# Kernel tuning notes

Hardware: AMD Instinct MI355X
Metric: run time of the kernel (lower is better)

## Reference

```python
import jax, jax.numpy as jnp
import numpy as np
import math

B, T, C = 4, 2048, 1024
H = 16
DH = C // H
SCALE = 1.0 / math.sqrt(DH)


def setup_inputs() -> dict:
    key = jax.random.key(0)
    k1, k2, k3 = jax.random.split(key, 3)
    x = jax.random.normal(k1, (B, T, C), dtype=jnp.float32)
    # init_unit_norm: randn / sqrt(d_in)
    W_qkv = jax.random.normal(k2, (3 * C, C), dtype=jnp.float32) / math.sqrt(C)
    W_out = jax.random.normal(k3, (C, C), dtype=jnp.float32) / math.sqrt(C)
    return {"x": x, "W_qkv": W_qkv, "W_out": W_out}


def reference(x, W_qkv, W_out):
    b, t, c = x.shape
    qkv = x @ W_qkv.T                      # [B,T,3C]
    q, k, v = jnp.split(qkv, 3, axis=-1)
    # [B,T,C] -> [B,H,T,Dh]
    q = q.reshape(b, t, H, DH).transpose(0, 2, 1, 3)
    k = k.reshape(b, t, H, DH).transpose(0, 2, 1, 3)
    v = v.reshape(b, t, H, DH).transpose(0, 2, 1, 3)
    scores = jnp.einsum('bhtd,bhsd->bhts', q, k) * SCALE  # [B,H,T,T]
    mask = jnp.tril(jnp.ones((t, t), dtype=bool))
    scores = jnp.where(mask, scores, 0.0)  # no softmax
    attn = jnp.einsum('bhts,bhsd->bhtd', scores, v)       # [B,H,T,Dh]
    attn = attn.transpose(0, 2, 1, 3).reshape(b, t, c)
    return attn @ W_out.T
```

## Files before the change

### kernel.cpp

```cpp
#include <hip/hip_runtime.h>

#define TT 2048
#define CC 1024

typedef __attribute__((ext_vector_type(8))) __bf16 bf16x8;
typedef __attribute__((ext_vector_type(4))) float f32x4;
typedef unsigned int u32;

__device__ __forceinline__ short f2bf(float f) {
  u32 u = __float_as_uint(f);
  u += 0x7fffu + ((u >> 16) & 1u);
  return (short)(u >> 16);
}

#if __has_builtin(__builtin_amdgcn_cvt_pk_bf16_f32)
__device__ __forceinline__ u32 pack2(float a, float b) {
  auto v = __builtin_amdgcn_cvt_pk_bf16_f32(a, b);
  return __builtin_bit_cast(u32, v);
}
#else
__device__ __forceinline__ u32 pack2(float a, float b) {
  u32 ua = __float_as_uint(a), ub = __float_as_uint(b);
  ua += 0x7fffu + ((ua >> 16) & 1u);
  ub += 0x7fffu + ((ub >> 16) & 1u);
  return (ua >> 16) | (ub & 0xffff0000u);
}
#endif

__global__ __launch_bounds__(256) void cvt_all(const float* __restrict__ x,
                                               const float* __restrict__ wqkv,
                                               const float* __restrict__ wout,
                                               short* __restrict__ dst) {
  int i = blockIdx.x * blockDim.x + threadIdx.x;
  const float* src;
  float sc = 1.0f;
  if (i < 2097152) {
    src = x + (size_t)i * 4;
  } else if (i < 2883584) {
    int j = i - 2097152;
    src = wqkv + (size_t)j * 4;
    if (j < 262144) sc = 0.125f;
  } else {
    src = wout + (size_t)(i - 2883584) * 4;
  }
  float4 f = *reinterpret_cast<const float4*>(src);
  short4 s;
  s.x = f2bf(f.x * sc); s.y = f2bf(f.y * sc); s.z = f2bf(f.z * sc); s.w = f2bf(f.w * sc);
  reinterpret_cast<short4*>(dst)[i] = s;
}

__device__ __forceinline__ void storev(float* p, float v) { *p = v; }
__device__ __forceinline__ void storev(short* p, float v) { *p = f2bf(v); }

#if __has_builtin(__builtin_amdgcn_global_load_lds)
#define HAVE_GLD_LDS 1
__device__ __forceinline__ void gld_lds16(const short* g, short* l) {
  __builtin_amdgcn_global_load_lds((const __attribute__((address_space(1))) u32*)g,
                                   (__attribute__((address_space(3))) u32*)l, 16, 0, 0);
}
#endif

__device__ __forceinline__ f32x4 mfma16(bf16x8 a, bf16x8 b, f32x4 c) {
  return __builtin_amdgcn_mfma_f32_16x16x32_bf16(a, b, c, 0, 0, 0);
}

template <int NN>
__device__ __forceinline__ void waitvm() {
  if constexpr (NN == 0) asm volatile("s_waitcnt vmcnt(0)" ::: "memory");
  else if constexpr (NN == 4) asm volatile("s_waitcnt vmcnt(4)" ::: "memory");
  else if constexpr (NN == 6) asm volatile("s_waitcnt vmcnt(6)" ::: "memory");
  else if constexpr (NN == 8) asm volatile("s_waitcnt vmcnt(8)" ::: "memory");
}

template <int MH, int NFR>
__device__ __forceinline__ void mmaN(f32x4 (&acc)[8][NFR], const bf16x8 (&af)[4],
                                     const bf16x8 (&bfr)[NFR]) {
#pragma unroll
  for (int mf = 0; mf < 4; ++mf)
#pragma unroll
    for (int nf = 0; nf < NFR; ++nf)
      acc[MH * 4 + mf][nf] = mfma16(af[mf], bfr[nf], acc[MH * 4 + mf][nf]);
}

#define GPHASE(DB, KS, MH, LOADB, STG, SYNC)               \
  {                                                        \
    ldA(af, DB, KS, MH);                                   \
    if (LOADB) ldB(bfr, DB, KS);                           \
    STG;                                                   \
    __builtin_amdgcn_s_setprio(1);                         \
    mmaN<MH>(acc, af, bfr);                                \
    __builtin_amdgcn_s_setprio(0);                         \
    asm volatile("s_waitcnt lgkmcnt(0)" ::: "memory");     \
    SYNC;                                                  \
    __builtin_amdgcn_s_barrier();                          \
  }
#define GNOOP ((void)0)

template <typename OutT, int N, int K, int BN, int RN>
__global__ __launch_bounds__(512, 2) void gemm8p(const short* __restrict__ A,
                                                 const short* __restrict__ B,
                                                 OutT* __restrict__ Cm) {
  constexpr int BGLD = BN / 128;
  constexpr int NFR = BN / 64;
  constexpr int SYNCN = 2 + 2 * BGLD;
  constexpr int NT = K / 64, NITER = NT / 2;
  constexpr int BHALF = BN * 32;
  constexpr int DBS = 16384 + BN * 64;
  extern __shared__ short lds[];
  const int tid = threadIdx.x;
  const int wave = tid >> 6, lane = tid & 63;
  const int quad = lane >> 4, nl = lane & 15;
  const int wm = wave >> 2, wn = wave & 3;

  const int id = blockIdx.x;
  const int xcd = id & 7, slot = id >> 3;
  const int mt = (xcd & 3) * 8 + (slot & 7);
  const int nt = (xcd >> 2) * RN + (slot >> 3);
  const int m0 = mt * 256, n0 = nt * BN;

  const int srow = lane >> 2;
  const int sperm = ((lane & 3) ^ ((lane >> 3) & 3)) * 8;
  const short* pA = A + (size_t)(m0 + wave * 32 + srow) * K + sperm;
  const short* pB = B + (size_t)(n0 + wave * (BN / 8) + srow) * K + sperm;

  const int perm = (quad ^ ((nl >> 1) & 3)) * 8;
  const int aoff = (wm * 128 + nl) * 32 + perm;
  const int boff = (wn * (BN / 4) + nl) * 32 + perm;

  f32x4 acc[8][NFR] = {};

  auto stageA = [&](int db, int ks, int t) {
    const short* s = pA + (size_t)t * 64 + ks * 32;
    short* d = lds + db * DBS + ks * 8192 + wave * 1024;
#if HAVE_GLD_LDS
    gld_lds16(s, d);
    gld_lds16(s + (size_t)16 * K, d + 512);
#else
    *reinterpret_cast<uint4*>(d + lane * 8) = *reinterpret_cast<const uint4*>(s);
    *reinterpret_cast<uint4*>(d + 512 + lane * 8) =
        *reinterpret_cast<const uint4*>(s + (size_t)16 * K);
#endif
  };
  auto stageB = [&](int db, int ks, int t) {
    const short* s = pB + (size_t)t * 64 + ks * 32;
    short* d = lds + db * DBS + 16384 + ks * BHALF + wave * (BN * 4);
#if HAVE_GLD_LDS
    gld_lds16(s, d);
    if constexpr (BGLD == 2) gld_lds16(s + (size_t)16 * K, d + 512);
#else
    *reinterpret_cast<uint4*>(d + lane * 8) = *reinterpret_cast<const uint4*>(s);
    if constexpr (BGLD == 2)
      *reinterpret_cast<uint4*>(d + 512 + lane * 8) =
          *reinterpret_cast<const uint4*>(s + (size_t)16 * K);
#endif
  };
  auto ldA = [&](bf16x8 (&af)[4], int db, int ks, int mh) {
#pragma unroll
    for (int mf = 0; mf < 4; ++mf)
      af[mf] = *reinterpret_cast<const bf16x8*>(
          &lds[db * DBS + ks * 8192 + aoff + (mh * 4 + mf) * 512]);
  };
  auto ldB = [&](bf16x8 (&bfr)[NFR], int db, int ks) {
#pragma unroll
    for (int nf = 0; nf < NFR; ++nf)
      bfr[nf] = *reinterpret_cast<const bf16x8*>(
          &lds[db * DBS + 16384 + ks * BHALF + boff + nf * 512]);
  };

  stageA(0, 0, 0); stageA(0, 1, 0); stageB(0, 0, 0); stageB(0, 1, 0);
  stageB(1, 0, 1); stageA(1, 0, 1); stageB(1, 1, 1);
  waitvm<SYNCN>();
  __builtin_amdgcn_s_barrier();

  for (int i = 0; i < NITER - 1; ++i) {
    const int to1 = 2 * i + 1, te2 = 2 * i + 2, to3 = 2 * i + 3;
    bf16x8 af[4], bfr[NFR];
    GPHASE(0, 0, 0, 1, stageA(1, 1, to1), GNOOP)
    GPHASE(0, 0, 1, 0, stageB(0, 0, te2), GNOOP)
    GPHASE(0, 1, 0, 1, stageA(0, 0, te2), GNOOP)
    GPHASE(0, 1, 1, 0, stageB(0, 1, te2), waitvm<SYNCN>())
    GPHASE(1, 0, 0, 1, stageA(0, 1, te2), GNOOP)
    GPHASE(1, 0, 1, 0, stageB(1, 0, to3), GNOOP)
    GPHASE(1, 1, 0, 1, stageA(1, 0, to3), GNOOP)
    GPHASE(1, 1, 1, 0, stageB(1, 1, to3), waitvm<SYNCN>())
  }
  {
    bf16x8 af[4], bfr[NFR];
    GPHASE(0, 0, 0, 1, stageA(1, 1, NT - 1), GNOOP)
    GPHASE(0, 0, 1, 0, GNOOP, GNOOP)
    GPHASE(0, 1, 0, 1, GNOOP, GNOOP)
    GPHASE(0, 1, 1, 0, GNOOP, waitvm<0>())
    GPHASE(1, 0, 0, 1, GNOOP, GNOOP)
    GPHASE(1, 0, 1, 0, GNOOP, GNOOP)
    GPHASE(1, 1, 0, 1, GNOOP, GNOOP)
    GPHASE(1, 1, 1, 0, GNOOP, GNOOP)
  }

#pragma unroll
  for (int mf = 0; mf < 8; ++mf) {
    const int row = m0 + wm * 128 + mf * 16 + quad * 4;
#pragma unroll
    for (int nf = 0; nf < NFR; ++nf) {
      const int col = n0 + wn * (BN / 4) + nf * 16 + nl;
#pragma unroll
      for (int r = 0; r < 4; ++r)
        storev(&Cm[(size_t)(row + r) * N + col], acc[mf][nf][r]);
    }
  }
}

__global__ __launch_bounds__(256) void transpose_v(const short* __restrict__ qkv,
                                                   short* __restrict__ vt) {
  __shared__ short Ls[64 * 68];
  const int bh = blockIdx.y, tb = blockIdx.x;
  const int b = bh >> 4, h = bh & 15;
  const int tid = threadIdx.x;
  const short* src = qkv + (size_t)(b * TT + tb * 64) * (3 * CC) + 2 * CC + h * 64;
#pragma unroll
  for (int i = 0; i < 2; ++i) {
    int idx = tid + i * 256;
    int tl = idx >> 3, dc = idx & 7;
    uint4 d4 = *reinterpret_cast<const uint4*>(&src[(size_t)tl * (3 * CC) + dc * 8]);
    *reinterpret_cast<uint2*>(&Ls[tl * 68 + dc * 8]) = make_uint2(d4.x, d4.y);
    *reinterpret_cast<uint2*>(&Ls[tl * 68 + dc * 8 + 4]) = make_uint2(d4.z, d4.w);
  }
  __syncthreads();
  short* dst = vt + (size_t)(bh * 64) * TT + tb * 64;
#pragma unroll
  for (int i = 0; i < 2; ++i) {
    int idx = tid + i * 256;
    int dl = idx >> 3, tc = idx & 7;
    short tmp[8];
#pragma unroll
    for (int j = 0; j < 8; ++j) tmp[j] = Ls[(tc * 8 + j) * 68 + dl];
    *reinterpret_cast<uint4*>(&dst[(size_t)dl * TT + tc * 8]) = *reinterpret_cast<uint4*>(tmp);
  }
}

template <bool DIAG>
__device__ __forceinline__ void attn_compute(const short* kf, const short* vf, u32* ssw,
                                             const bf16x8 (&qf)[2][2], f32x4 (&o)[2][4],
                                             int lane, int quad, int nl) {
  bf16x8 k00 = *reinterpret_cast<const bf16x8*>(&kf[0 * 512 + lane * 8]);
  bf16x8 k01 = *reinterpret_cast<const bf16x8*>(&kf[1 * 512 + lane * 8]);
  bf16x8 k10 = *reinterpret_cast<const bf16x8*>(&kf[2 * 512 + lane * 8]);
  bf16x8 k11 = *reinterpret_cast<const bf16x8*>(&kf[3 * 512 + lane * 8]);
  bf16x8 vB[4];
#pragma unroll
  for (int nb = 0; nb < 4; ++nb)
    vB[nb] = *reinterpret_cast<const bf16x8*>(&vf[nb * 512 + lane * 8]);
  {
    u32* srow = &ssw[0 * 320 + nl * 20];
    f32x4 s0 = {};
    s0 = mfma16(k00, qf[0][0], s0);
    s0 = mfma16(k01, qf[0][1], s0);
    if (DIAG) {
#pragma unroll
      for (int r = 0; r < 4; ++r) s0[r] = (quad * 4 + r <= nl) ? s0[r] : 0.0f;
    }
#pragma unroll
    for (int p = 0; p < 2; ++p) srow[quad * 2 + p] = pack2(s0[2 * p], s0[2 * p + 1]);
    if (DIAG) {
#pragma unroll
      for (int p = 0; p < 2; ++p) srow[8 + quad * 2 + p] = 0;
    } else {
      f32x4 s1 = {};
      s1 = mfma16(k10, qf[0][0], s1);
      s1 = mfma16(k11, qf[0][1], s1);
#pragma unroll
      for (int p = 0; p < 2; ++p) srow[8 + quad * 2 + p] = pack2(s1[2 * p], s1[2 * p + 1]);
    }
  }
  {
    u32* srow = &ssw[1 * 320 + nl * 20];
    f32x4 s0 = {}, s1 = {};
    s0 = mfma16(k00, qf[1][0], s0);
    s0 = mfma16(k01, qf[1][1], s0);
    s1 = mfma16(k10, qf[1][0], s1);
    s1 = mfma16(k11, qf[1][1], s1);
    if (DIAG) {
#pragma unroll
      for (int r = 0; r < 4; ++r) s1[r] = (quad * 4 + r <= nl) ? s1[r] : 0.0f;
    }
#pragma unroll
    for (int p = 0; p < 2; ++p) {
      srow[quad * 2 + p] = pack2(s0[2 * p], s0[2 * p + 1]);
      srow[8 + quad * 2 + p] = pack2(s1[2 * p], s1[2 * p + 1]);
    }
  }
#pragma unroll
  for (int m = 0; m < 2; ++m) {
    bf16x8 sf = *reinterpret_cast<const bf16x8*>(&ssw[m * 320 + nl * 20 + quad * 4]);
#pragma unroll
    for (int nb = 0; nb < 4; ++nb) o[m][nb] = mfma16(sf, vB[nb], o[m][nb]);
  }
}

__global__ __launch_bounds__(256, 3) void attn_kernel(const short* __restrict__ qkv,
                                                      const short* __restrict__ vt,
                                                      short* __restrict__ attnb) {
  const int bh = blockIdx.x;
  const int b = bh >> 4, h = bh & 15;
  const int ti = 15 - blockIdx.y;
  const int T0 = ti * 128;
  const int tid = threadIdx.x;
  const int wave = tid >> 6, lane = tid & 63;
  const int quad = lane >> 4, nl = lane & 15;

  const short* qbase = qkv + (size_t)(b * TT) * (3 * CC) + h * 64;
  const short* kbase = qbase + CC;
  const short* vbase = vt + (size_t)(bh * 64) * TT;

  __shared__ __align__(16) short Frag[2][8192];
  __shared__ __align__(16) u32 Ss[4][640];
  u32* ssw = Ss[wave];

  const int tw0 = T0 + wave * 32;
  bf16x8 qf[2][2];
#pragma unroll
  for (int m = 0; m < 2; ++m)
#pragma unroll
    for (int half = 0; half < 2; ++half)
      qf[m][half] = *reinterpret_cast<const bf16x8*>(
          &qbase[(size_t)(tw0 + m * 16 + nl) * (3 * CC) + half * 32 + quad * 8]);

  f32x4 o[2][4] = {};

  const short* ksrc = kbase + (size_t)(wave * 16 + nl) * (3 * CC) + quad * 8;
  const int sp_w = wave >> 1, nb0 = (wave & 1) * 2;
  const short* vsrc0 = vbase + (size_t)((nb0 + 0) * 16 + nl) * TT + sp_w * 32 + quad * 8;
  const short* vsrc1 = vbase + (size_t)((nb0 + 1) * 16 + nl) * TT + sp_w * 32 + quad * 8;

  auto stage = [&](short* fb, int c) {
    const size_t koff = (size_t)(c * 64) * (3 * CC);
#if HAVE_GLD_LDS
    gld_lds16(ksrc + koff, &fb[(2 * wave) * 512]);
    gld_lds16(ksrc + koff + 32, &fb[(2 * wave + 1) * 512]);
    gld_lds16(vsrc0 + c * 64, &fb[4096 + (2 * wave) * 512]);
    gld_lds16(vsrc1 + c * 64, &fb[4096 + (2 * wave + 1) * 512]);
#else
    *reinterpret_cast<uint4*>(&fb[(2 * wave) * 512 + lane * 8]) =
        *reinterpret_cast<const uint4*>(ksrc + koff);
    *reinterpret_cast<uint4*>(&fb[(2 * wave + 1) * 512 + lane * 8]) =
        *reinterpret_cast<const uint4*>(ksrc + koff + 32);
    *reinterpret_cast<uint4*>(&fb[4096 + (2 * wave) * 512 + lane * 8]) =
        *reinterpret_cast<const uint4*>(vsrc0 + c * 64);
    *reinterpret_cast<uint4*>(&fb[4096 + (2 * wave + 1) * 512 + lane * 8]) =
        *reinterpret_cast<const uint4*>(vsrc1 + c * 64);
#endif
  };

  const int nch = 2 * ti + 2;
  const int cd = 4 * ti + wave;

  stage(Frag[0], 0);
  for (int c = 0; c < nch; ++c) {
    __syncthreads();
    if (c + 1 < nch) stage(Frag[(c + 1) & 1], c + 1);
    const short* fb = Frag[c & 1];
    const int c0 = 2 * c, c1 = 2 * c + 1;
    if (c0 < cd)
      attn_compute<false>(fb, fb + 4096, ssw, qf, o, lane, quad, nl);
    else if (c0 == cd)
      attn_compute<true>(fb, fb + 4096, ssw, qf, o, lane, quad, nl);
    if (c1 < cd)
      attn_compute<false>(fb + 2048, fb + 4096 + 2048, ssw, qf, o, lane, quad, nl);
    else if (c1 == cd)
      attn_compute<true>(fb + 2048, fb + 4096 + 2048, ssw, qf, o, lane, quad, nl);
  }

#pragma unroll
  for (int m = 0; m < 2; ++m)
#pragma unroll
    for (int nb = 0; nb < 4; ++nb)
#pragma unroll
      for (int r = 0; r < 4; ++r) {
        int t = tw0 + m * 16 + quad * 4 + r;
        attnb[(size_t)(b * TT + t) * CC + h * 64 + nb * 16 + nl] = f2bf(o[m][nb][r]);
      }
}

extern "C" void kernel_launch(void* const* d_in, const int* in_sizes, int n_in,
                              void* d_out, int out_size, void* d_ws, size_t ws_size,
                              hipStream_t stream) {
  const float* x = (const float*)d_in[0];
  const float* wqkv = (const float*)d_in[1];
  const float* wout = (const float*)d_in[2];
  float* out = (float*)d_out;

  char* ws = (char*)d_ws;
  short* xb    = (short*)(ws);
  short* wqkvb = (short*)(ws + 16777216);
  short* woutb = (short*)(ws + 23068672);
  short* qkvb  = (short*)(ws + 25165824);
  short* attnb = (short*)(ws + 75497472);
  short* vt    = xb;

  static bool inited = false;
  if (!inited) {
    hipFuncSetAttribute(reinterpret_cast<const void*>(&gemm8p<short, 3072, 1024, 256, 6>),
                        hipFuncAttributeMaxDynamicSharedMemorySize, 131072);
    hipFuncSetAttribute(reinterpret_cast<const void*>(&gemm8p<float, 1024, 1024, 128, 4>),
                        hipFuncAttributeMaxDynamicSharedMemorySize, 98304);
    inited = true;
  }

  cvt_all<<<12288, 256, 0, stream>>>(x, wqkv, wout, xb);

  gemm8p<short, 3072, 1024, 256, 6><<<384, 512, 131072, stream>>>(xb, wqkvb, qkvb);

  transpose_v<<<dim3(32, 64), 256, 0, stream>>>(qkvb, vt);

  attn_kernel<<<dim3(64, 16), 256, 0, stream>>>(qkvb, vt, attnb);

  gemm8p<float, 1024, 1024, 128, 4><<<256, 512, 98304, stream>>>(attnb, woutb, out);
}
```

Measured before the change: 238.2 us.

## Replace 8-phase GEMM with 4-phase generic BMxBN tile pipeline

Rewrites the GEMM kernel into a generic BM×BN tiled version that uses four pipeline phases per iteration, each loading the full A and B fragments and waiting on outstanding loads every phase. The old eight-phase kernel split M into halves. The QKV projection now uses 128×384 tiles on 512 blocks, and the output projection uses 128×256 tiles, changing grid shape and per-block reuse. The larger N-tile raises register pressure from the accumulators, and the more frequent vmcnt waits may reduce the overlap between loads and compute.

```diff
diff --git a/kernel.cpp b/kernel.cpp
--- a/kernel.cpp
+++ b/kernel.cpp
@@ -67,45 +67,40 @@
 template <int NN>
 __device__ __forceinline__ void waitvm() {
   if constexpr (NN == 0) asm volatile("s_waitcnt vmcnt(0)" ::: "memory");
+  else if constexpr (NN == 3) asm volatile("s_waitcnt vmcnt(3)" ::: "memory");
   else if constexpr (NN == 4) asm volatile("s_waitcnt vmcnt(4)" ::: "memory");
   else if constexpr (NN == 6) asm volatile("s_waitcnt vmcnt(6)" ::: "memory");
   else if constexpr (NN == 8) asm volatile("s_waitcnt vmcnt(8)" ::: "memory");
 }
 
-template <int MH, int NFR>
-__device__ __forceinline__ void mmaN(f32x4 (&acc)[8][NFR], const bf16x8 (&af)[4],
-                                     const bf16x8 (&bfr)[NFR]) {
-#pragma unroll
-  for (int mf = 0; mf < 4; ++mf)
-#pragma unroll
-    for (int nf = 0; nf < NFR; ++nf)
-      acc[MH * 4 + mf][nf] = mfma16(af[mf], bfr[nf], acc[MH * 4 + mf][nf]);
-}
-
-#define GPHASE(DB, KS, MH, LOADB, STG, SYNC)               \
+#define GNOOP ((void)0)
+#define GPHASE4(DB, KS, STG, SYNC)                         \
   {                                                        \
-    ldA(af, DB, KS, MH);                                   \
-    if (LOADB) ldB(bfr, DB, KS);                           \
+    bf16x8 af[MFRAG], bfr[NFR];                            \
+    ldA(af, DB, KS);                                       \
+    ldB(bfr, DB, KS);                                      \
     STG;                                                   \
     __builtin_amdgcn_s_setprio(1);                         \
-    mmaN<MH>(acc, af, bfr);                                \
+    mmaAll(af, bfr);                                       \
     __builtin_amdgcn_s_setprio(0);                         \
     asm volatile("s_waitcnt lgkmcnt(0)" ::: "memory");     \
     SYNC;                                                  \
     __builtin_amdgcn_s_barrier();                          \
   }
-#define GNOOP ((void)0)
-
-template <typename OutT, int N, int K, int BN, int RN>
-__global__ __launch_bounds__(512, 2) void gemm8p(const short* __restrict__ A,
+
+template <typename OutT, int N, int K, int BM, int BN>
+__global__ __launch_bounds__(512, 2) void gemm4p(const short* __restrict__ A,
                                                  const short* __restrict__ B,
                                                  OutT* __restrict__ Cm) {
+  constexpr int MFRAG = BM / 32;
+  constexpr int NFR = BN / 64;
+  constexpr int AGLD = BM / 128;
   constexpr int BGLD = BN / 128;
-  constexpr int NFR = BN / 64;
-  constexpr int SYNCN = 2 + 2 * BGLD;
+  constexpr int GPP = AGLD + BGLD;
+  constexpr int SYNCN = 2 * GPP;
   constexpr int NT = K / 64, NITER = NT / 2;
-  constexpr int BHALF = BN * 32;
-  constexpr int DBS = 16384 + BN * 64;
+  constexpr int DBS = 64 * (BM + BN);
+  constexpr int TMX = (8192 / BM) / 8;
   extern __shared__ short lds[];
   const int tid = threadIdx.x;
   const int wave = tid >> 6, lane = tid & 63;
@@ -114,91 +109,85 @@
 
   const int id = blockIdx.x;
   const int xcd = id & 7, slot = id >> 3;
-  const int mt = (xcd & 3) * 8 + (slot & 7);
-  const int nt = (xcd >> 2) * RN + (slot >> 3);
-  const int m0 = mt * 256, n0 = nt * BN;
+  const int mt = xcd * TMX + (slot % TMX);
+  const int nt = slot / TMX;
+  const int m0 = mt * BM, n0 = nt * BN;
 
   const int srow = lane >> 2;
   const int sperm = ((lane & 3) ^ ((lane >> 3) & 3)) * 8;
-  const short* pA = A + (size_t)(m0 + wave * 32 + srow) * K + sperm;
+  const short* pA = A + (size_t)(m0 + wave * (BM / 8) + srow) * K + sperm;
   const short* pB = B + (size_t)(n0 + wave * (BN / 8) + srow) * K + sperm;
 
   const int perm = (quad ^ ((nl >> 1) & 3)) * 8;
-  const int aoff = (wm * 128 + nl) * 32 + perm;
-  const int boff = (wn * (BN / 4) + nl) * 32 + perm;
-
-  f32x4 acc[8][NFR] = {};
+
+  f32x4 acc[MFRAG][NFR] = {};
 
   auto stageA = [&](int db, int ks, int t) {
     const short* s = pA + (size_t)t * 64 + ks * 32;
-    short* d = lds + db * DBS + ks * 8192 + wave * 1024;
+    short* d = lds + db * DBS + ks * (BM * 32) + wave * (BM * 4);
+#pragma unroll
+    for (int j = 0; j < AGLD; ++j) {
 #if HAVE_GLD_LDS
-    gld_lds16(s, d);
-    gld_lds16(s + (size_t)16 * K, d + 512);
+      gld_lds16(s + (size_t)j * 16 * K, d + j * 512);
 #else
-    *reinterpret_cast<uint4*>(d + lane * 8) = *reinterpret_cast<const uint4*>(s);
-    *reinterpret_cast<uint4*>(d + 512 + lane * 8) =
-        *reinterpret_cast<const uint4*>(s + (size_t)16 * K);
+      *reinterpret_cast<uint4*>(d + j * 512 + lane * 8) =
+          *reinterpret_cast<const uint4*>(s + (size_t)j * 16 * K);
 #endif
+    }
   };
   auto stageB = [&](int db, int ks, int t) {
     const short* s = pB + (size_t)t * 64 + ks * 32;
-    short* d = lds + db * DBS + 16384 + ks * BHALF + wave * (BN * 4);
+    short* d = lds + db * DBS + BM * 64 + ks * (BN * 32) + wave * (BN * 4);
+#pragma unroll
+    for (int j = 0; j < BGLD; ++j) {
 #if HAVE_GLD_LDS
-    gld_lds16(s, d);
-    if constexpr (BGLD == 2) gld_lds16(s + (size_t)16 * K, d + 512);
+      gld_lds16(s + (size_t)j * 16 * K, d + j * 512);
 #else
-    *reinterpret_cast<uint4*>(d + lane * 8) = *reinterpret_cast<const uint4*>(s);
-    if constexpr (BGLD == 2)
-      *reinterpret_cast<uint4*>(d + 512 + lane * 8) =
-          *reinterpret_cast<const uint4*>(s + (size_t)16 * K);
+      *reinterpret_cast<uint4*>(d + j * 512 + lane * 8) =
+          *reinterpret_cast<const uint4*>(s + (size_t)j * 16 * K);
 #endif
-  };
-  auto ldA = [&](bf16x8 (&af)[4], int db, int ks, int mh) {
-#pragma unroll
-    for (int mf = 0; mf < 4; ++mf)
+    }
+  };
+  auto stage = [&](int db, int ks, int t) { stageA(db, ks, t); stageB(db, ks, t); };
+
+  auto ldA = [&](bf16x8 (&af)[MFRAG], int db, int ks) {
+#pragma unroll
+    for (int mf = 0; mf < MFRAG; ++mf)
       af[mf] = *reinterpret_cast<const bf16x8*>(
-          &lds[db * DBS + ks * 8192 + aoff + (mh * 4 + mf) * 512]);
+          &lds[db * DBS + ks * (BM * 32) + (wm * (BM / 2) + mf * 16 + nl) * 32 + perm]);
   };
   auto ldB = [&](bf16x8 (&bfr)[NFR], int db, int ks) {
 #pragma unroll
     for (int nf = 0; nf < NFR; ++nf)
       bfr[nf] = *reinterpret_cast<const bf16x8*>(
-          &lds[db * DBS + 16384 + ks * BHALF + boff + nf * 512]);
-  };
-
-  stageA(0, 0, 0); stageA(0, 1, 0); stageB(0, 0, 0); stageB(0, 1, 0);
-  stageB(1, 0, 1); stageA(1, 0, 1); stageB(1, 1, 1);
+          &lds[db * DBS + BM * 64 + ks * (BN * 32) + (wn * (BN / 4) + nf * 16 + nl) * 32 + perm]);
+  };
+  auto mmaAll = [&](const bf16x8 (&af)[MFRAG], const bf16x8 (&bfr)[NFR]) {
+#pragma unroll
+    for (int mf = 0; mf < MFRAG; ++mf)
+#pragma unroll
+      for (int nf = 0; nf < NFR; ++nf)
+        acc[mf][nf] = mfma16(af[mf], bfr[nf], acc[mf][nf]);
+  };
+
+  stage(0, 0, 0); stage(0, 1, 0); stage(1, 0, 1);
   waitvm<SYNCN>();
   __builtin_amdgcn_s_barrier();
 
   for (int i = 0; i < NITER - 1; ++i) {
-    const int to1 = 2 * i + 1, te2 = 2 * i + 2, to3 = 2 * i + 3;
-    bf16x8 af[4], bfr[NFR];
-    GPHASE(0, 0, 0, 1, stageA(1, 1, to1), GNOOP)
-    GPHASE(0, 0, 1, 0, stageB(0, 0, te2), GNOOP)
-    GPHASE(0, 1, 0, 1, stageA(0, 0, te2), GNOOP)
-    GPHASE(0, 1, 1, 0, stageB(0, 1, te2), waitvm<SYNCN>())
-    GPHASE(1, 0, 0, 1, stageA(0, 1, te2), GNOOP)
-    GPHASE(1, 0, 1, 0, stageB(1, 0, to3), GNOOP)
-    GPHASE(1, 1, 0, 1, stageA(1, 0, to3), GNOOP)
-    GPHASE(1, 1, 1, 0, stageB(1, 1, to3), waitvm<SYNCN>())
-  }
-  {
-    bf16x8 af[4], bfr[NFR];
-    GPHASE(0, 0, 0, 1, stageA(1, 1, NT - 1), GNOOP)
-    GPHASE(0, 0, 1, 0, GNOOP, GNOOP)
-    GPHASE(0, 1, 0, 1, GNOOP, GNOOP)
-    GPHASE(0, 1, 1, 0, GNOOP, waitvm<0>())
-    GPHASE(1, 0, 0, 1, GNOOP, GNOOP)
-    GPHASE(1, 0, 1, 0, GNOOP, GNOOP)
-    GPHASE(1, 1, 0, 1, GNOOP, GNOOP)
-    GPHASE(1, 1, 1, 0, GNOOP, GNOOP)
-  }
-
-#pragma unroll
-  for (int mf = 0; mf < 8; ++mf) {
-    const int row = m0 + wm * 128 + mf * 16 + quad * 4;
+    GPHASE4(0, 0, stage(1, 1, 2 * i + 1), waitvm<SYNCN>())
+    GPHASE4(0, 1, stage(0, 0, 2 * i + 2), waitvm<SYNCN>())
+    GPHASE4(1, 0, stage(0, 1, 2 * i + 2), waitvm<SYNCN>())
+    GPHASE4(1, 1, stage(1, 0, 2 * i + 3), waitvm<SYNCN>())
+  }
+  GPHASE4(0, 0, stage(1, 1, NT - 1), waitvm<SYNCN>())
+  GPHASE4(0, 1, GNOOP, waitvm<GPP>())
+  GPHASE4(1, 0, GNOOP, waitvm<0>())
+  GPHASE4(1, 1, GNOOP, GNOOP)
+
+#pragma unroll
+  for (int mf = 0; mf < MFRAG; ++mf) {
+    const int row = m0 + wm * (BM / 2) + mf * 16 + quad * 4;
 #pragma unroll
     for (int nf = 0; nf < NFR; ++nf) {
       const int col = n0 + wn * (BN / 4) + nf * 16 + nl;
@@ -398,20 +387,20 @@
 
   static bool inited = false;
   if (!inited) {
-    hipFuncSetAttribute(reinterpret_cast<const void*>(&gemm8p<short, 3072, 1024, 256, 6>),
+    hipFuncSetAttribute(reinterpret_cast<const void*>(&gemm4p<short, 3072, 1024, 128, 384>),
                         hipFuncAttributeMaxDynamicSharedMemorySize, 131072);
-    hipFuncSetAttribute(reinterpret_cast<const void*>(&gemm8p<float, 1024, 1024, 128, 4>),
+    hipFuncSetAttribute(reinterpret_cast<const void*>(&gemm4p<float, 1024, 1024, 128, 256>),
                         hipFuncAttributeMaxDynamicSharedMemorySize, 98304);
     inited = true;
   }
 
   cvt_all<<<12288, 256, 0, stream>>>(x, wqkv, wout, xb);
 
-  gemm8p<short, 3072, 1024, 256, 6><<<384, 512, 131072, stream>>>(xb, wqkvb, qkvb);
+  gemm4p<short, 3072, 1024, 128, 384><<<512, 512, 131072, stream>>>(xb, wqkvb, qkvb);
 
   transpose_v<<<dim3(32, 64), 256, 0, stream>>>(qkvb, vt);
 
   attn_kernel<<<dim3(64, 16), 256, 0, stream>>>(qkvb, vt, attnb);
 
-  gemm8p<float, 1024, 1024, 128, 4><<<256, 512, 98304, stream>>>(attnb, woutb, out);
-}
+  gemm4p<float, 1024, 1024, 128, 256><<<256, 512, 98304, stream>>>(attnb, woutb, out);
+}
```

Result: faster. 232.0 us (-2.6%).
